# Kernel optimization log

Hardware: AMD Instinct MI355X
Metric: run time of the kernel (lower is better)

## Reference

```python
import jax, jax.numpy as jnp
import numpy as np
from jax import lax

E, D, I, K = 8, 1024, 2048, 2
B, S = 4, 1024


def setup_inputs() -> dict:
    key = jax.random.key(0)
    k1, k2, k3, k4, k5 = jax.random.split(key, 5)
    x = jax.random.normal(k1, (B, S, D), dtype=jnp.float32)
    routing_weights = jax.random.uniform(k2, (B, S, K), dtype=jnp.float32)
    selected_experts = jax.random.randint(k3, (B, S, K), 0, E).astype(jnp.int64)
    w1 = 0.02 * jax.random.normal(k4, (E, D, I), dtype=jnp.float32)
    w2 = 0.02 * jax.random.normal(k5, (E, I, D), dtype=jnp.float32)
    return {"x": x, "routing_weights": routing_weights,
            "selected_experts": selected_experts, "w1": w1, "w2": w2}


def reference(x, routing_weights, selected_experts, w1, w2):
    shape = x.shape
    d = shape[-1]
    xf = x.reshape(-1, d)                       # [T, D]
    rw = routing_weights.reshape(xf.shape[0], -1)   # [T, K]
    se = selected_experts.reshape(xf.shape[0], -1)  # [T, K]
    n_experts = w1.shape[0]

    def body(acc, inputs):
        e, w1e, w2e = inputs
        # per-token combine weight for expert e (rw assumed >= 0; zero weight == not routed)
        wt = jnp.sum(jnp.where(se == e, rw, 0.0), axis=-1)  # [T]
        h = jax.nn.silu(xf @ w1e)                # [T, I]
        out = h @ w2e                            # [T, D]
        return acc + out * wt[:, None], None

    acc0 = jnp.zeros_like(xf)
    acc, _ = lax.scan(body, acc0, (jnp.arange(n_experts), w1, w2))
    return acc.reshape(shape)
```

## Files before the change

### kernel.cpp

```cpp
#include <hip/hip_runtime.h>
#include <stdint.h>

#define E_EXPERTS 8
#define D_DIM 1024
#define I_DIM 2048
#define T_TOKENS 4096
#define NSLOTS 8192
#define TILE 128
#define MAXPAD (NSLOTS + E_EXPERTS * TILE)
#define TPX 9

#define W1_TILES (E_EXPERTS * (D_DIM / 32) * (I_DIM / 32))
#define W2_TILES W1_TILES
#define CX_BLOCKS (T_TOKENS * D_DIM / 1024)
#define PREP_GRID (1 + W1_TILES + W2_TILES + CX_BLOCKS)

typedef __attribute__((ext_vector_type(8))) short bf16x8;
typedef __attribute__((ext_vector_type(4))) float f32x4;

__device__ __forceinline__ unsigned short f2b(float f) {
  union { float f; uint32_t u; } v; v.f = f;
  uint32_t r = v.u + 0x7FFFu + ((v.u >> 16) & 1u);
  return (unsigned short)(r >> 16);
}
__device__ __forceinline__ float b2f(unsigned short u) {
  union { uint32_t u; float f; } v; v.u = ((uint32_t)u) << 16; return v.f;
}

__device__ __forceinline__ void async16(const unsigned short* g, unsigned short* l) {
  __builtin_amdgcn_global_load_lds(
      (const __attribute__((address_space(1))) void*)g,
      (__attribute__((address_space(3))) void*)l, 16, 0, 0);
}

__global__ __launch_bounds__(256) void prep_k(
    const float* __restrict__ x, const float* __restrict__ w1, const float* __restrict__ w2,
    const int* __restrict__ se,
    unsigned short* __restrict__ xb, unsigned short* __restrict__ w1t,
    unsigned short* __restrict__ w2t,
    int* __restrict__ ntiles, int* __restrict__ desc,
    int* __restrict__ tok, int* __restrict__ slot_of) {
  int b = blockIdx.x;
  int tid = threadIdx.x;

  if (b == 0) {
    __shared__ int scnt[E_EXPERTS], sbase[E_EXPERTS + 1], scur[E_EXPERTS];
    if (tid < E_EXPERTS) scnt[tid] = 0;
    __syncthreads();
    for (int s = tid; s < NSLOTS; s += 256) atomicAdd(&scnt[se[s]], 1);
    __syncthreads();
    if (tid == 0) {
      int acc = 0, nt = 0;
      for (int e = 0; e < E_EXPERTS; e++) {
        int n = scnt[e];
        sbase[e] = acc;
        scur[e] = acc;
        int pad = (n + TILE - 1) & ~(TILE - 1);
        for (int m = 0; m * TILE < pad; m++) { desc[2 * nt] = e; desc[2 * nt + 1] = acc + m * TILE; nt++; }
        acc += pad;
      }
      sbase[E_EXPERTS] = acc;
      *ntiles = nt;
    }
    __syncthreads();
    for (int e = 0; e < E_EXPERTS; e++) {
      int s0 = sbase[e] + scnt[e], s1 = sbase[e + 1];
      for (int s = s0 + tid; s < s1; s += 256) tok[s] = 0;
    }
    for (int s = tid; s < NSLOTS; s += 256) {
      int e = se[s];
      int pos = atomicAdd(&scur[e], 1);
      tok[pos] = s >> 1;
      slot_of[s] = pos;
    }
    return;
  }

  if (b > W1_TILES + W2_TILES) {
    int cb = b - 1 - W1_TILES - W2_TILES;
    int i = (cb * 256 + tid) * 4;
    float4 v = *(const float4*)(x + i);
    ushort4 o;
    o.x = f2b(v.x); o.y = f2b(v.y); o.z = f2b(v.z); o.w = f2b(v.w);
    *(ushort4*)(xb + i) = o;
    return;
  }

  __shared__ float t[32][33];
  const float* src; unsigned short* dst; int R, C, id;
  if (b <= W1_TILES) { id = b - 1;            src = w1; dst = w1t; R = D_DIM; C = I_DIM; }
  else               { id = b - 1 - W1_TILES; src = w2; dst = w2t; R = I_DIM; C = D_DIM; }
  int eid = id >> 11;
  int tt = id & 2047;
  int ctiles = C / 32;
  int c0 = (tt % ctiles) * 32, r0 = (tt / ctiles) * 32;
  size_t eoff = (size_t)eid * R * C;
  int tx = tid & 7, ty = tid >> 3;
  float4 v = *(const float4*)(src + eoff + (size_t)(r0 + ty) * C + c0 + tx * 4);
  t[ty][tx * 4 + 0] = v.x; t[ty][tx * 4 + 1] = v.y;
  t[ty][tx * 4 + 2] = v.z; t[ty][tx * 4 + 3] = v.w;
  __syncthreads();
  ushort4 o;
  o.x = f2b(t[tx * 4 + 0][ty]); o.y = f2b(t[tx * 4 + 1][ty]);
  o.z = f2b(t[tx * 4 + 2][ty]); o.w = f2b(t[tx * 4 + 3][ty]);
  *(ushort4*)(dst + eoff + (size_t)(c0 + ty) * R + r0 + tx * 4) = o;
}

template <int KLEN, int ASTR, int BSTR, int NDIM, int PHASE>
__global__ __launch_bounds__(256) void moe_gemm_k(
    const unsigned short* __restrict__ Amat, const unsigned short* __restrict__ Bt,
    const int* __restrict__ desc, const int* __restrict__ ntiles_p,
    const int* __restrict__ tok, unsigned short* __restrict__ Hout) {
  int id = blockIdx.x;
  int xcd = id & 7, r = id >> 3;
  int ti = xcd * TPX + r % TPX;
  int q = r / TPX;
  int nb, kh;
  if (PHASE == 1) { nb = q; kh = 0; }
  else           { kh = q & 1; nb = q >> 1; }
  if (ti >= *ntiles_p) return;
  int e = desc[2 * ti];
  int slot0 = desc[2 * ti + 1];

  const unsigned short* Bbase = Bt + (size_t)e * NDIM * BSTR + (size_t)nb * 128 * BSTR + kh * KLEN;

  __shared__ unsigned short As[128 * 64];
  __shared__ unsigned short Bs[128 * 64];

  int tid = threadIdx.x;
  int lane = tid & 63;
  int wave = tid >> 6;
  int wm = (wave >> 1) * 64, wn = (wave & 1) * 64;
  int l15 = lane & 15, quad = lane >> 4;

  f32x4 acc[4][4] = {};

  int sr = tid >> 3;
  int ldoff = (((lane & 7) ^ (lane >> 3)) * 8);

  const unsigned short* arow[4];
  const unsigned short* brow[4];
#pragma unroll
  for (int p = 0; p < 4; p++) {
    int rr = sr + p * 32;
    int row = (PHASE == 1) ? tok[slot0 + rr] : (slot0 + rr);
    arow[p] = Amat + (size_t)row * ASTR + kh * KLEN + ldoff;
    brow[p] = Bbase + (size_t)rr * BSTR + ldoff;
  }

  for (int kt = 0; kt < KLEN / 64; kt++) {
    int k0 = kt * 64;
#pragma unroll
    for (int p = 0; p < 4; p++) {
      unsigned short* adst = As + (size_t)(p * 256 + wave * 64) * 8;
      unsigned short* bdst = Bs + (size_t)(p * 256 + wave * 64) * 8;
      async16(arow[p] + k0, adst);
      async16(brow[p] + k0, bdst);
    }
    __syncthreads();
#pragma unroll
    for (int ks = 0; ks < 2; ks++) {
      bf16x8 af[4], bfr[4];
#pragma unroll
      for (int i = 0; i < 4; i++) {
        int rr = wm + i * 16 + l15;
        int cc = (((ks * 4 + quad) ^ (rr & 7)) * 8);
        af[i] = *(const bf16x8*)&As[rr * 64 + cc];
      }
#pragma unroll
      for (int j = 0; j < 4; j++) {
        int rr = wn + j * 16 + l15;
        int cc = (((ks * 4 + quad) ^ (rr & 7)) * 8);
        bfr[j] = *(const bf16x8*)&Bs[rr * 64 + cc];
      }
#pragma unroll
      for (int i = 0; i < 4; i++)
#pragma unroll
        for (int j = 0; j < 4; j++)
          acc[i][j] = __builtin_amdgcn_mfma_f32_16x16x32_bf16(af[i], bfr[j], acc[i][j], 0, 0, 0);
    }
    __syncthreads();
  }

#pragma unroll
  for (int i = 0; i < 4; i++) {
    int slotr = slot0 + wm + i * 16 + quad * 4;
#pragma unroll
    for (int rg = 0; rg < 4; rg++) {
      int row = slotr + rg;
      size_t base = (PHASE == 1) ? (size_t)row * NDIM
                                 : ((size_t)kh * MAXPAD + row) * NDIM;
#pragma unroll
      for (int j = 0; j < 4; j++) {
        int col = nb * 128 + wn + j * 16 + l15;
        float v = acc[i][j][rg];
        if (PHASE == 1) v = v / (1.f + __expf(-v));
        Hout[base + col] = f2b(v);
      }
    }
  }
}

__global__ void combine_k(const unsigned short* __restrict__ y, const float* __restrict__ rw,
                          const int* __restrict__ slot_of, float* __restrict__ out) {
  int g = blockIdx.x * blockDim.x + threadIdx.x;
  int t = g >> 7, dd = (g & 127) * 8;
  int s0 = slot_of[2 * t], s1 = slot_of[2 * t + 1];
  float w0 = rw[2 * t], w1 = rw[2 * t + 1];
  const unsigned short* p00 = y + (size_t)s0 * D_DIM + dd;
  const unsigned short* p01 = y + ((size_t)MAXPAD + s0) * D_DIM + dd;
  const unsigned short* p10 = y + (size_t)s1 * D_DIM + dd;
  const unsigned short* p11 = y + ((size_t)MAXPAD + s1) * D_DIM + dd;
  ushort4 a0 = *(const ushort4*)p00, a1 = *(const ushort4*)(p00 + 4);
  ushort4 b0 = *(const ushort4*)p01, b1 = *(const ushort4*)(p01 + 4);
  ushort4 c0 = *(const ushort4*)p10, c1 = *(const ushort4*)(p10 + 4);
  ushort4 d0 = *(const ushort4*)p11, d1 = *(const ushort4*)(p11 + 4);
  float4 o0, o1;
  o0.x = w0 * (b2f(a0.x) + b2f(b0.x)) + w1 * (b2f(c0.x) + b2f(d0.x));
  o0.y = w0 * (b2f(a0.y) + b2f(b0.y)) + w1 * (b2f(c0.y) + b2f(d0.y));
  o0.z = w0 * (b2f(a0.z) + b2f(b0.z)) + w1 * (b2f(c0.z) + b2f(d0.z));
  o0.w = w0 * (b2f(a0.w) + b2f(b0.w)) + w1 * (b2f(c0.w) + b2f(d0.w));
  o1.x = w0 * (b2f(a1.x) + b2f(b1.x)) + w1 * (b2f(c1.x) + b2f(d1.x));
  o1.y = w0 * (b2f(a1.y) + b2f(b1.y)) + w1 * (b2f(c1.y) + b2f(d1.y));
  o1.z = w0 * (b2f(a1.z) + b2f(b1.z)) + w1 * (b2f(c1.z) + b2f(d1.z));
  o1.w = w0 * (b2f(a1.w) + b2f(b1.w)) + w1 * (b2f(c1.w) + b2f(d1.w));
  float* op = out + (size_t)t * D_DIM + dd;
  *(float4*)op = o0;
  *(float4*)(op + 4) = o1;
}

extern "C" void kernel_launch(void* const* d_in, const int* in_sizes, int n_in,
                              void* d_out, int out_size, void* d_ws, size_t ws_size,
                              hipStream_t stream) {
  (void)in_sizes; (void)n_in; (void)ws_size; (void)out_size;
  const float* x  = (const float*)d_in[0];
  const float* rw = (const float*)d_in[1];
  const int*   se = (const int*)d_in[2];
  const float* w1 = (const float*)d_in[3];
  const float* w2 = (const float*)d_in[4];
  float* out = (float*)d_out;
  char* ws = (char*)d_ws;

  int* ntiles  = (int*)(ws + 128);
  int* desc    = (int*)(ws + 256);
  int* tok     = (int*)(ws + 4096);
  int* slot_of = (int*)(ws + 40960);
  unsigned short* xb   = (unsigned short*)(ws + 131072);
  unsigned short* w1t  = xb + (size_t)T_TOKENS * D_DIM;
  unsigned short* w2t  = w1t + (size_t)E_EXPERTS * D_DIM * I_DIM;
  unsigned short* hbuf = w2t + (size_t)E_EXPERTS * D_DIM * I_DIM;
  unsigned short* ypart = xb;

  prep_k<<<PREP_GRID, 256, 0, stream>>>(x, w1, w2, se, xb, w1t, w2t,
                                        ntiles, desc, tok, slot_of);
  moe_gemm_k<1024, 1024, 1024, I_DIM, 1><<<8 * TPX * (I_DIM / 128), 256, 0, stream>>>(
      xb, w1t, desc, ntiles, tok, hbuf);
  moe_gemm_k<1024, 2048, 2048, D_DIM, 2><<<8 * TPX * (D_DIM / 128) * 2, 256, 0, stream>>>(
      hbuf, w2t, desc, ntiles, tok, ypart);

  combine_k<<<T_TOKENS * 128 / 256, 256, 0, stream>>>(ypart, rw, slot_of, out);
}
```

Before: 290.4 us.

## Overlap w2 transpose-convert with first expert GEMM and use 64x64 transpose tiles

The w2 fp32→bf16 transpose moves out of the prep kernel and into the first GEMM launch, interleaved 1:4 by block id with the GEMM blocks. The aim is to hide the bandwidth-bound conversion behind the compute-bound GEMM1. Transpose tiles grow from 32x32 to 64x64 with 16-byte bf16 stores, and the x conversion does 4 float4 per thread. This cuts block count and store granularity overhead, at the cost of a larger LDS union and more complex block scheduling.

```diff
diff --git a/kernel.cpp b/kernel.cpp
--- a/kernel.cpp
+++ b/kernel.cpp
@@ -10,13 +10,16 @@
 #define MAXPAD (NSLOTS + E_EXPERTS * TILE)
 #define TPX 9
 
-#define W1_TILES (E_EXPERTS * (D_DIM / 32) * (I_DIM / 32))
-#define W2_TILES W1_TILES
-#define CX_BLOCKS (T_TOKENS * D_DIM / 1024)
-#define PREP_GRID (1 + W1_TILES + W2_TILES + CX_BLOCKS)
+#define W1_TT 4096
+#define W2_TT 4096
+#define CX_BLOCKS 1024
+#define PREP_GRID (1 + W1_TT + CX_BLOCKS)
+#define NG1 (8 * TPX * (I_DIM / 128))
+#define G1_GRID (NG1 * 5)
 
 typedef __attribute__((ext_vector_type(8))) short bf16x8;
 typedef __attribute__((ext_vector_type(4))) float f32x4;
+typedef __attribute__((ext_vector_type(8))) unsigned short u16x8;
 
 __device__ __forceinline__ unsigned short f2b(float f) {
   union { float f; uint32_t u; } v; v.f = f;
@@ -33,11 +36,39 @@
       (__attribute__((address_space(3))) void*)l, 16, 0, 0);
 }
 
-__global__ __launch_bounds__(256) void prep_k(
-    const float* __restrict__ x, const float* __restrict__ w1, const float* __restrict__ w2,
+__device__ __forceinline__ void tile_tr64(const float* __restrict__ src,
+                                          unsigned short* __restrict__ dst,
+                                          int R, int C, int t, int tid,
+                                          float (*lt)[65]) {
+  int eid = t >> 9, tt = t & 511;
+  int ctiles = C >> 6;
+  int c0 = (tt % ctiles) << 6, r0 = (tt / ctiles) << 6;
+  size_t eoff = (size_t)eid * R * C;
+  int tx = tid & 15, ty = tid >> 4;
+#pragma unroll
+  for (int q = 0; q < 4; q++) {
+    float4 v = *(const float4*)(src + eoff + (size_t)(r0 + ty + q * 16) * C + c0 + tx * 4);
+    lt[ty + q * 16][tx * 4 + 0] = v.x;
+    lt[ty + q * 16][tx * 4 + 1] = v.y;
+    lt[ty + q * 16][tx * 4 + 2] = v.z;
+    lt[ty + q * 16][tx * 4 + 3] = v.w;
+  }
+  __syncthreads();
+  int ox = tid & 7, oy = tid >> 3;
+#pragma unroll
+  for (int q = 0; q < 2; q++) {
+    int cr = oy + q * 32;
+    u16x8 o;
+#pragma unroll
+    for (int j = 0; j < 8; j++) o[j] = f2b(lt[ox * 8 + j][cr]);
+    *(u16x8*)(dst + eoff + (size_t)(c0 + cr) * R + r0 + ox * 8) = o;
+  }
+}
+
+__global__ __launch_bounds__(256) void prep_a_k(
+    const float* __restrict__ x, const float* __restrict__ w1,
     const int* __restrict__ se,
     unsigned short* __restrict__ xb, unsigned short* __restrict__ w1t,
-    unsigned short* __restrict__ w2t,
     int* __restrict__ ntiles, int* __restrict__ desc,
     int* __restrict__ tok, int* __restrict__ slot_of) {
   int b = blockIdx.x;
@@ -76,56 +107,41 @@
     return;
   }
 
-  if (b > W1_TILES + W2_TILES) {
-    int cb = b - 1 - W1_TILES - W2_TILES;
-    int i = (cb * 256 + tid) * 4;
+  if (b <= W1_TT) {
+    __shared__ float lt[64][65];
+    tile_tr64(w1, w1t, D_DIM, I_DIM, b - 1, tid, lt);
+    return;
+  }
+
+  int cb = b - 1 - W1_TT;
+  int base = cb * 4096 + tid * 4;
+#pragma unroll
+  for (int q = 0; q < 4; q++) {
+    int i = base + q * 1024;
     float4 v = *(const float4*)(x + i);
     ushort4 o;
     o.x = f2b(v.x); o.y = f2b(v.y); o.z = f2b(v.z); o.w = f2b(v.w);
     *(ushort4*)(xb + i) = o;
-    return;
-  }
-
-  __shared__ float t[32][33];
-  const float* src; unsigned short* dst; int R, C, id;
-  if (b <= W1_TILES) { id = b - 1;            src = w1; dst = w1t; R = D_DIM; C = I_DIM; }
-  else               { id = b - 1 - W1_TILES; src = w2; dst = w2t; R = I_DIM; C = D_DIM; }
-  int eid = id >> 11;
-  int tt = id & 2047;
-  int ctiles = C / 32;
-  int c0 = (tt % ctiles) * 32, r0 = (tt / ctiles) * 32;
-  size_t eoff = (size_t)eid * R * C;
-  int tx = tid & 7, ty = tid >> 3;
-  float4 v = *(const float4*)(src + eoff + (size_t)(r0 + ty) * C + c0 + tx * 4);
-  t[ty][tx * 4 + 0] = v.x; t[ty][tx * 4 + 1] = v.y;
-  t[ty][tx * 4 + 2] = v.z; t[ty][tx * 4 + 3] = v.w;
-  __syncthreads();
-  ushort4 o;
-  o.x = f2b(t[tx * 4 + 0][ty]); o.y = f2b(t[tx * 4 + 1][ty]);
-  o.z = f2b(t[tx * 4 + 2][ty]); o.w = f2b(t[tx * 4 + 3][ty]);
-  *(ushort4*)(dst + eoff + (size_t)(c0 + ty) * R + r0 + tx * 4) = o;
+  }
 }
 
 template <int KLEN, int ASTR, int BSTR, int NDIM, int PHASE>
-__global__ __launch_bounds__(256) void moe_gemm_k(
+__device__ __forceinline__ void gemm_body(
     const unsigned short* __restrict__ Amat, const unsigned short* __restrict__ Bt,
     const int* __restrict__ desc, const int* __restrict__ ntiles_p,
-    const int* __restrict__ tok, unsigned short* __restrict__ Hout) {
-  int id = blockIdx.x;
-  int xcd = id & 7, r = id >> 3;
+    const int* __restrict__ tok, unsigned short* __restrict__ Hout,
+    int xcd, int r, int kh_in, unsigned short* As, unsigned short* Bs) {
   int ti = xcd * TPX + r % TPX;
   int q = r / TPX;
   int nb, kh;
   if (PHASE == 1) { nb = q; kh = 0; }
   else           { kh = q & 1; nb = q >> 1; }
+  (void)kh_in;
   if (ti >= *ntiles_p) return;
   int e = desc[2 * ti];
   int slot0 = desc[2 * ti + 1];
 
   const unsigned short* Bbase = Bt + (size_t)e * NDIM * BSTR + (size_t)nb * 128 * BSTR + kh * KLEN;
-
-  __shared__ unsigned short As[128 * 64];
-  __shared__ unsigned short Bs[128 * 64];
 
   int tid = threadIdx.x;
   int lane = tid & 63;
@@ -199,6 +215,38 @@
       }
     }
   }
+}
+
+__global__ __launch_bounds__(256) void gemm1_fused_k(
+    const unsigned short* __restrict__ xb, const unsigned short* __restrict__ w1t,
+    const float* __restrict__ w2, unsigned short* __restrict__ w2t,
+    const int* __restrict__ desc, const int* __restrict__ ntiles_p,
+    const int* __restrict__ tok, unsigned short* __restrict__ hbuf) {
+  __shared__ union {
+    struct { unsigned short As[128 * 64]; unsigned short Bs[128 * 64]; } g;
+    float lt[64][65];
+  } sm;
+  int id = blockIdx.x;
+  int m5 = id % 5;
+  if (m5 == 0) {
+    int gid = id / 5;
+    gemm_body<1024, 1024, 1024, I_DIM, 1>(xb, w1t, desc, ntiles_p, tok, hbuf,
+                                          id & 7, gid >> 3, 0, sm.g.As, sm.g.Bs);
+  } else {
+    int t = id - id / 5 - 1;
+    if (t < W2_TT) tile_tr64(w2, w2t, I_DIM, D_DIM, t, threadIdx.x, sm.lt);
+  }
+}
+
+__global__ __launch_bounds__(256) void gemm2_k(
+    const unsigned short* __restrict__ hbuf, const unsigned short* __restrict__ w2t,
+    const int* __restrict__ desc, const int* __restrict__ ntiles_p,
+    const int* __restrict__ tok, unsigned short* __restrict__ ypart) {
+  __shared__ unsigned short As[128 * 64];
+  __shared__ unsigned short Bs[128 * 64];
+  int id = blockIdx.x;
+  gemm_body<1024, 2048, 2048, D_DIM, 2>(hbuf, w2t, desc, ntiles_p, tok, ypart,
+                                        id & 7, id >> 3, 0, As, Bs);
 }
 
 __global__ void combine_k(const unsigned short* __restrict__ y, const float* __restrict__ rw,
@@ -251,12 +299,8 @@
   unsigned short* hbuf = w2t + (size_t)E_EXPERTS * D_DIM * I_DIM;
   unsigned short* ypart = xb;
 
-  prep_k<<<PREP_GRID, 256, 0, stream>>>(x, w1, w2, se, xb, w1t, w2t,
-                                        ntiles, desc, tok, slot_of);
-  moe_gemm_k<1024, 1024, 1024, I_DIM, 1><<<8 * TPX * (I_DIM / 128), 256, 0, stream>>>(
-      xb, w1t, desc, ntiles, tok, hbuf);
-  moe_gemm_k<1024, 2048, 2048, D_DIM, 2><<<8 * TPX * (D_DIM / 128) * 2, 256, 0, stream>>>(
-      hbuf, w2t, desc, ntiles, tok, ypart);
-
+  prep_a_k<<<PREP_GRID, 256, 0, stream>>>(x, w1, se, xb, w1t, ntiles, desc, tok, slot_of);
+  gemm1_fused_k<<<G1_GRID, 256, 0, stream>>>(xb, w1t, w2, w2t, desc, ntiles, tok, hbuf);
+  gemm2_k<<<8 * TPX * (D_DIM / 128) * 2, 256, 0, stream>>>(hbuf, w2t, desc, ntiles, tok, ypart);
   combine_k<<<T_TOKENS * 128 / 256, 256, 0, stream>>>(ypart, rw, slot_of, out);
 }
```

Result: slower. 318.1 us (+9.5%).
